# Kernel optimization log

Hardware: AMD Instinct MI355X
Metric: run time of the kernel (lower is better)

## Reference

```python
import jax, jax.numpy as jnp
import numpy as np

N, H, D, G = 8192, 512, 256, 64
TAU, LAM, ALPHA, BETA = 0.5, 0.5, 1.0, 1.0
EPS_G, EPS_L = 1e-6, 1e-5


def setup_inputs() -> dict:
    key = jax.random.key(0)
    ks = jax.random.split(key, 8)
    za = jax.random.normal(ks[0], (N, H), dtype=jnp.float32)
    zb = jax.random.normal(ks[1], (N, H), dtype=jnp.float32)
    pos = jax.random.uniform(ks[2], (N, N), dtype=jnp.float32)
    batch = (jnp.arange(N, dtype=jnp.int32) * G) // N  # sorted, covers all G groups
    s_h = np.sqrt(2.0 / H).astype(np.float32)  # kaiming fan_in relu
    W1 = jax.random.normal(ks[3], (H, H), dtype=jnp.float32) * s_h
    b1 = jnp.zeros((H,), dtype=jnp.float32)
    W2 = jax.random.normal(ks[4], (H, H), dtype=jnp.float32) * s_h
    b2 = jnp.zeros((H,), dtype=jnp.float32)
    W3 = jax.random.normal(ks[5], (H, D), dtype=jnp.float32) * s_h
    b3 = jnp.zeros((D,), dtype=jnp.float32)
    a1 = jnp.full((1,), 0.5, dtype=jnp.float32)
    g1 = jnp.ones((H,), dtype=jnp.float32)
    be1 = jnp.zeros((H,), dtype=jnp.float32)
    a2 = jnp.full((1,), 0.5, dtype=jnp.float32)
    g2 = jnp.ones((H,), dtype=jnp.float32)
    be2 = jnp.zeros((H,), dtype=jnp.float32)
    return {"za": za, "zb": zb, "pos": pos, "batch": batch,
            "W1": W1, "b1": b1, "a1": a1, "g1": g1, "be1": be1,
            "W2": W2, "b2": b2, "a2": a2, "g2": g2, "be2": be2,
            "W3": W3, "b3": b3}


def _project(z, W1, b1, a1, g1, be1, W2, b2, a2, g2, be2, W3, b3):
    h = z @ W1 + b1
    h = jnp.tanh(a1 * h) * g1 + be1  # DyT
    h = h @ W2 + b2
    h = jnp.tanh(a2 * h) * g2 + be2  # DyT
    p = h @ W3 + b3
    return p * jax.nn.sigmoid(p)  # z1_proj * sigmoid(z1_proj)


def reference(za, zb, pos, batch, W1, b1, a1, g1, be1, W2, b2, a2, g2, be2, W3, b3):
    za_p = _project(za, W1, b1, a1, g1, be1, W2, b2, a2, g2, be2, W3, b3)
    zb_p = _project(zb, W1, b1, a1, g1, be1, W2, b2, a2, g2, be2, W3, b3)

    # exp(cosine / tau): same matrix used by global_contrast (sim) and local_contrast
    na = jnp.linalg.norm(za_p, axis=-1, keepdims=True)  # [N,1]
    nb = jnp.linalg.norm(zb_p, axis=-1, keepdims=True)  # [N,1]
    m = jnp.exp((za_p @ zb_p.T) / (na * nb.T) / TAU)    # [N,N]

    # global contrast
    a2b = m / (jnp.sum(m, axis=1, keepdims=True) + EPS_G)
    lori_a = -jnp.mean(jnp.log(jnp.sum(a2b * pos, axis=-1)))
    b2a = m.T
    b2a = b2a / (jnp.sum(b2a, axis=1, keepdims=True) + EPS_G)
    lori_b = -jnp.mean(jnp.log(jnp.sum(b2a * pos, axis=-1)))
    global_loss = LAM * lori_a + (1.0 - LAM) * lori_b

    # local contrast: per-group sums via one-hot matmul (replaces O(G^2) mask loop)
    pos_sim = jnp.diagonal(m)                              # [N]
    pos_sim_graph = jax.ops.segment_sum(pos_sim, batch, num_segments=G)  # [G]
    hot = jax.nn.one_hot(batch, G, dtype=m.dtype)          # [N,G]
    batch_sim = hot.T @ m @ hot                            # [G,G]
    graph_sim = jnp.diagonal(batch_sim)
    neg0 = jnp.sum(batch_sim, axis=0) - graph_sim
    neg1 = jnp.sum(batch_sim, axis=1) - graph_sim
    loss0 = jnp.mean(jnp.log(pos_sim_graph / (neg0 + EPS_L)))
    loss1 = jnp.mean(jnp.log(pos_sim_graph / (neg1 + EPS_L)))
    inter_loss = (loss0 + loss1) / 2.0
    inner_loss = -jnp.mean(jnp.log(pos_sim_graph / (graph_sim - pos_sim_graph + EPS_L)))
    local_loss = ALPHA * inter_loss + BETA * inner_loss

    total_loss = global_loss + local_loss
    return total_loss, jnp.concatenate((za_p, zb_p), axis=1)
```

## Files before the change

kernel.cpp:

```cpp
#include <hip/hip_runtime.h>
#include <hip/hip_bf16.h>
#include <cstdint>
#include <cstddef>


typedef __bf16 bf16;
typedef __bf16 bf16x4 __attribute__((ext_vector_type(4)));
typedef __bf16 bf16x8 __attribute__((ext_vector_type(8)));
typedef float  f32x4  __attribute__((ext_vector_type(4)));

#define NROWS 8192
#define HDIM  512
#define DDIM  256
#define GGRP  64
#define INV_TAU 2.0f

__device__ __forceinline__ void async_ld16(const void* g, void* l) {
    __builtin_amdgcn_global_load_lds(
        (__attribute__((address_space(1))) void*)(g),
        (__attribute__((address_space(3))) void*)(l), 16, 0, 0);
}

__device__ __forceinline__ void mfma_tile_128(
    const bf16* __restrict__ A, const bf16* __restrict__ Bt, int K,
    int row0, int col0, bf16* ldsA, bf16* ldsB, f32x4 acc[4][4], int tid)
{
    const int lane = tid & 63;
    const int wave = tid >> 6;
    const int wrow = (wave >> 1) * 64;
    const int wcol = (wave & 1) * 64;
    const int lrow = lane & 15;
    const int lk8  = (lane >> 4) * 8;

    const int sr = tid >> 2;
    const int sc = (tid & 3) * 8;
    const bf16* gA0 = A  + (size_t)(row0 + sr) * K + sc;
    const bf16* gA1 = gA0 + (size_t)64 * K;
    const bf16* gB0 = Bt + (size_t)(col0 + sr) * K + sc;
    const bf16* gB1 = gB0 + (size_t)64 * K;
    bf16* dA0 = ldsA + (wave * 64) * 8;
    bf16* dA1 = ldsA + (256 + wave * 64) * 8;
    bf16* dB0 = ldsB + (wave * 64) * 8;
    bf16* dB1 = ldsB + (256 + wave * 64) * 8;

#pragma unroll
    for (int i = 0; i < 4; i++)
#pragma unroll
        for (int j = 0; j < 4; j++) acc[i][j] = (f32x4){0.f, 0.f, 0.f, 0.f};

    for (int k0 = 0; k0 < K; k0 += 32) {
        async_ld16(gA0, dA0); async_ld16(gA1, dA1);
        async_ld16(gB0, dB0); async_ld16(gB1, dB1);
        gA0 += 32; gA1 += 32; gB0 += 32; gB1 += 32;
        __syncthreads();

        bf16x8 af[4], bfr[4];
#pragma unroll
        for (int fi = 0; fi < 4; fi++)
            af[fi] = *(const bf16x8*)(ldsA + (wrow + fi * 16 + lrow) * 32 + lk8);
#pragma unroll
        for (int fj = 0; fj < 4; fj++)
            bfr[fj] = *(const bf16x8*)(ldsB + (wcol + fj * 16 + lrow) * 32 + lk8);
#pragma unroll
        for (int fi = 0; fi < 4; fi++)
#pragma unroll
            for (int fj = 0; fj < 4; fj++)
                acc[fi][fj] = __builtin_amdgcn_mfma_f32_16x16x32_bf16(
                    af[fi], bfr[fj], acc[fi][fj], 0, 0, 0);
        __syncthreads();
    }
}

__global__ __launch_bounds__(256) void gemm_dyt(
    const bf16* __restrict__ A, const bf16* __restrict__ Bt, bf16* __restrict__ C,
    int K, int N,
    const float* __restrict__ bias, const float* __restrict__ alph,
    const float* __restrict__ gam, const float* __restrict__ bet)
{
    __shared__ __align__(16) bf16 ldsA[128 * 32];
    __shared__ __align__(16) bf16 ldsB[128 * 32];
    f32x4 acc[4][4];
    const int row0 = blockIdx.y * 128, col0 = blockIdx.x * 128;
    mfma_tile_128(A, Bt, K, row0, col0, ldsA, ldsB, acc, threadIdx.x);

    const int lane = threadIdx.x & 63, wave = threadIdx.x >> 6;
    const int wrow = (wave >> 1) * 64, wcol = (wave & 1) * 64;
    const int lcol = lane & 15, lrg = (lane >> 4) * 4;
    const float a = alph[0];
#pragma unroll
    for (int fi = 0; fi < 4; fi++) {
        const int rbase = row0 + wrow + fi * 16 + lrg;
#pragma unroll
        for (int fj = 0; fj < 4; fj++) {
            const int cg = col0 + wcol + fj * 16 + lcol;
            const float bcol = bias[cg], gcol = gam[cg], becol = bet[cg];
#pragma unroll
            for (int r = 0; r < 4; r++) {
                float x = acc[fi][fj][r] + bcol;
                float y = tanhf(a * x) * gcol + becol;
                C[(size_t)(rbase + r) * N + cg] = (bf16)y;
            }
        }
    }
}

__global__ __launch_bounds__(256) void gemm_silu(
    const bf16* __restrict__ A, const bf16* __restrict__ Bt,
    bf16* __restrict__ P16, float* __restrict__ out1, float* __restrict__ n2,
    const float* __restrict__ bias)
{
    __shared__ __align__(16) bf16 ldsA[128 * 32];
    __shared__ __align__(16) bf16 ldsB[128 * 32];
    f32x4 acc[4][4];
    const int row0 = blockIdx.y * 128, col0 = blockIdx.x * 128;
    mfma_tile_128(A, Bt, 512, row0, col0, ldsA, ldsB, acc, threadIdx.x);

    const int lane = threadIdx.x & 63, wave = threadIdx.x >> 6;
    const int wrow = (wave >> 1) * 64, wcol = (wave & 1) * 64;
    const int lcol = lane & 15, lrg = (lane >> 4) * 4;

    float nacc[4][4];
#pragma unroll
    for (int i = 0; i < 4; i++)
#pragma unroll
        for (int r = 0; r < 4; r++) nacc[i][r] = 0.f;

#pragma unroll
    for (int fi = 0; fi < 4; fi++) {
        const int rbase = row0 + wrow + fi * 16 + lrg;
#pragma unroll
        for (int fj = 0; fj < 4; fj++) {
            const int cg = col0 + wcol + fj * 16 + lcol;
            const float bcol = bias[cg];
#pragma unroll
            for (int r = 0; r < 4; r++) {
                const int rg = rbase + r;
                float x = acc[fi][fj][r] + bcol;
                float y = x / (1.f + __expf(-x));
                P16[(size_t)rg * 256 + cg] = (bf16)y;
                size_t oidx = (rg < NROWS) ? ((size_t)rg * 512 + cg)
                                           : ((size_t)(rg - NROWS) * 512 + 256 + cg);
                out1[oidx] = y;
                nacc[fi][r] += y * y;
            }
        }
    }
#pragma unroll
    for (int fi = 0; fi < 4; fi++)
#pragma unroll
        for (int r = 0; r < 4; r++) {
            float v = nacc[fi][r];
            v += __shfl_xor(v, 1); v += __shfl_xor(v, 2);
            v += __shfl_xor(v, 4); v += __shfl_xor(v, 8);
            if (lcol == 0)
                atomicAdd(&n2[row0 + wrow + fi * 16 + lrg + r], v);
        }
}

template <int PASS1>
__global__ __launch_bounds__(256, 2) void sim_pass(
    const bf16* __restrict__ PA, const bf16* __restrict__ PB,
    const float* __restrict__ rnA, const float* __restrict__ rnB,
    const float* __restrict__ pos,
    float* __restrict__ rsum, float* __restrict__ wsum,
    float* __restrict__ bsim, float* __restrict__ psg)
{
    __shared__ __align__(16) bf16  ldsA[128 * 32];
    __shared__ __align__(16) bf16  ldsB[128 * 32];
    __shared__ __align__(16) float ldsP[128 * 128];

    const int tid  = threadIdx.x;
    const int lane = tid & 63, wave = tid >> 6;
    const int wrow = (wave >> 1) * 64, wcol = (wave & 1) * 64;
    const int lrow = lane & 15, lk8 = (lane >> 4) * 8;
    const int I = blockIdx.y, J = blockIdx.x;
    const int row0 = I * 128, col0 = J * 128;

    const int sr = tid >> 2, sc = (tid & 3) * 8;
    const bf16* gA0 = PA + (size_t)(row0 + sr) * DDIM + sc;
    const bf16* gA1 = gA0 + (size_t)64 * DDIM;
    const bf16* gB0 = PB + (size_t)(col0 + sr) * DDIM + sc;
    const bf16* gB1 = gB0 + (size_t)64 * DDIM;
    bf16* dA0 = ldsA + (wave * 64) * 8;
    bf16* dA1 = ldsA + (256 + wave * 64) * 8;
    bf16* dB0 = ldsB + (wave * 64) * 8;
    bf16* dB1 = ldsB + (256 + wave * 64) * 8;

    const int pr0 = tid >> 5;
    const int pc0 = (tid & 31) * 4;
    const float* gP0 = pos + (size_t)(row0 + pr0) * NROWS + col0 + pc0;
    const float* gP1 = gP0 + (size_t)8 * NROWS;
    float* dP = ldsP + wave * 256;

    f32x4 acc[4][4];
#pragma unroll
    for (int i = 0; i < 4; i++)
#pragma unroll
        for (int j = 0; j < 4; j++) acc[i][j] = (f32x4){0.f, 0.f, 0.f, 0.f};

    for (int it = 0; it < 8; ++it) {
        async_ld16(gA0, dA0); async_ld16(gA1, dA1);
        async_ld16(gB0, dB0); async_ld16(gB1, dB1);
        async_ld16(gP0, dP);  async_ld16(gP1, dP + 1024);
        gA0 += 32; gA1 += 32; gB0 += 32; gB1 += 32;
        gP0 += (size_t)16 * NROWS; gP1 += (size_t)16 * NROWS; dP += 2048;
        __syncthreads();

        bf16x8 af[4], bfr[4];
#pragma unroll
        for (int fi = 0; fi < 4; fi++)
            af[fi] = *(const bf16x8*)(ldsA + (wrow + fi * 16 + lrow) * 32 + lk8);
#pragma unroll
        for (int fj = 0; fj < 4; fj++)
            bfr[fj] = *(const bf16x8*)(ldsB + (wcol + fj * 16 + lrow) * 32 + lk8);
#pragma unroll
        for (int fi = 0; fi < 4; fi++)
#pragma unroll
            for (int fj = 0; fj < 4; fj++)
                acc[fi][fj] = __builtin_amdgcn_mfma_f32_16x16x32_bf16(
                    af[fi], bfr[fj], acc[fi][fj], 0, 0, 0);
        __syncthreads();
    }

    const int lcol = lane & 15, lrg = (lane >> 4) * 4;
    float racc[4][4], sacc[4][4];
#pragma unroll
    for (int i = 0; i < 4; i++)
#pragma unroll
        for (int r = 0; r < 4; r++) { racc[i][r] = 0.f; sacc[i][r] = 0.f; }
    float msum = 0.f;

#pragma unroll
    for (int fi = 0; fi < 4; fi++) {
        const int rl = wrow + fi * 16 + lrg;
        const int rbase = row0 + rl;
        float rna[4];
#pragma unroll
        for (int r = 0; r < 4; r++) rna[r] = rnA[rbase + r] * INV_TAU;
#pragma unroll
        for (int fj = 0; fj < 4; fj++) {
            const int cl = wcol + fj * 16 + lcol;
            const int cg = col0 + cl;
            const float rnb = rnB[cg];
#pragma unroll
            for (int r = 0; r < 4; r++) {
                float mval = __expf(acc[fi][fj][r] * rna[r] * rnb);
                float pv = ldsP[(rl + r) * 128 + cl];
                racc[fi][r] += mval;
                sacc[fi][r] += mval * pv;
                if (PASS1) {
                    msum += mval;
                    if (I == J && (rbase + r) == cg)
                        atomicAdd(&psg[I], mval);
                }
            }
        }
    }
#pragma unroll
    for (int fi = 0; fi < 4; fi++)
#pragma unroll
        for (int r = 0; r < 4; r++) {
            float rv = racc[fi][r], sv = sacc[fi][r];
            rv += __shfl_xor(rv, 1); rv += __shfl_xor(rv, 2);
            rv += __shfl_xor(rv, 4); rv += __shfl_xor(rv, 8);
            sv += __shfl_xor(sv, 1); sv += __shfl_xor(sv, 2);
            sv += __shfl_xor(sv, 4); sv += __shfl_xor(sv, 8);
            if (lcol == 0) {
                const int rg = row0 + wrow + fi * 16 + lrg + r;
                atomicAdd(&rsum[rg], rv);
                atomicAdd(&wsum[rg], sv);
            }
        }
    if (PASS1) {
        msum += __shfl_xor(msum, 1);  msum += __shfl_xor(msum, 2);
        msum += __shfl_xor(msum, 4);  msum += __shfl_xor(msum, 8);
        msum += __shfl_xor(msum, 16); msum += __shfl_xor(msum, 32);
        if (lane == 0) atomicAdd(&bsim[I * GGRP + J], msum);
    }
}

__global__ void cast4_kernel(const float4* __restrict__ x, bf16x4* __restrict__ y, int n4)
{
    int i = blockIdx.x * blockDim.x + threadIdx.x;
    if (i < n4) {
        float4 v = x[i];
        bf16x4 o;
        o[0] = (bf16)v.x; o[1] = (bf16)v.y; o[2] = (bf16)v.z; o[3] = (bf16)v.w;
        y[i] = o;
    }
}

__global__ void transpose_cast(const float* __restrict__ W, bf16* __restrict__ Wt,
                               int R, int C)
{
    __shared__ float tile[32][33];
    const int c0 = blockIdx.x * 32, r0 = blockIdx.y * 32;
    const int tx = threadIdx.x, ty = threadIdx.y;
    for (int i = ty; i < 32; i += 8)
        tile[i][tx] = W[(size_t)(r0 + i) * C + c0 + tx];
    __syncthreads();
    for (int i = ty; i < 32; i += 8)
        Wt[(size_t)(c0 + i) * R + r0 + tx] = (bf16)tile[tx][i];
}

__global__ void rsqrt_kernel(const float* __restrict__ x, float* __restrict__ y, int n)
{
    int i = blockIdx.x * blockDim.x + threadIdx.x;
    if (i < n) y[i] = rsqrtf(fmaxf(x[i], 1e-30f));
}

__global__ __launch_bounds__(256) void loss_rows(
    const float* __restrict__ sa, const float* __restrict__ rowsum,
    const float* __restrict__ sb, const float* __restrict__ colsum,
    float* __restrict__ gsum)
{
    __shared__ float red[8];
    const int i = blockIdx.x * 256 + threadIdx.x;
    float la = __logf(sa[i] / (rowsum[i] + 1e-6f));
    float lb = __logf(sb[i] / (colsum[i] + 1e-6f));
    for (int m = 1; m < 64; m <<= 1) { la += __shfl_xor(la, m); lb += __shfl_xor(lb, m); }
    const int w = threadIdx.x >> 6;
    if ((threadIdx.x & 63) == 0) { red[w] = la; red[4 + w] = lb; }
    __syncthreads();
    if (threadIdx.x == 0)  atomicAdd(&gsum[0], red[0] + red[1] + red[2] + red[3]);
    if (threadIdx.x == 64) atomicAdd(&gsum[1], red[4] + red[5] + red[6] + red[7]);
}

__global__ void loss_final(
    const float* __restrict__ bs, const float* __restrict__ psg,
    const float* __restrict__ gsum, float* __restrict__ out)
{
    const int t = threadIdx.x;
    float c0 = 0.f, c1 = 0.f;
    for (int a = 0; a < GGRP; a++) { c0 += bs[a * GGRP + t]; c1 += bs[t * GGRP + a]; }
    const float d = bs[t * (GGRP + 1)];
    const float p = psg[t];
    float l0  = __logf(p / (c0 - d + 1e-5f));
    float l1  = __logf(p / (c1 - d + 1e-5f));
    float lin = __logf(p / (d - p + 1e-5f));
    for (int m = 1; m < 64; m <<= 1) {
        l0 += __shfl_xor(l0, m); l1 += __shfl_xor(l1, m); lin += __shfl_xor(lin, m);
    }
    if (t == 0) {
        const float lori_a = -gsum[0] / (float)NROWS;
        const float lori_b = -gsum[1] / (float)NROWS;
        const float global_loss = 0.5f * (lori_a + lori_b);
        const float inter = 0.5f * (l0 + l1) / (float)GGRP;
        const float inner = -lin / (float)GGRP;
        out[0] = global_loss + inter + inner;
    }
}

extern "C" void kernel_launch(void* const* d_in, const int* in_sizes, int n_in,
                              void* d_out, int out_size, void* d_ws, size_t ws_size,
                              hipStream_t stream)
{
    const float* za  = (const float*)d_in[0];
    const float* zb  = (const float*)d_in[1];
    const float* pos = (const float*)d_in[2];
    const float* W1  = (const float*)d_in[4];
    const float* b1  = (const float*)d_in[5];
    const float* a1  = (const float*)d_in[6];
    const float* g1  = (const float*)d_in[7];
    const float* be1 = (const float*)d_in[8];
    const float* W2  = (const float*)d_in[9];
    const float* b2  = (const float*)d_in[10];
    const float* a2  = (const float*)d_in[11];
    const float* g2  = (const float*)d_in[12];
    const float* be2 = (const float*)d_in[13];
    const float* W3  = (const float*)d_in[14];
    const float* b3  = (const float*)d_in[15];
    float* out = (float*)d_out;

    char* ws = (char*)d_ws;
    float* rowsum = (float*)(ws);
    float* colsum = rowsum + 8192;
    float* s_a    = colsum + 8192;
    float* s_b    = s_a + 8192;
    float* n2     = s_b + 8192;
    float* bsim   = n2 + 16384;
    float* psg    = bsim + 4096;
    float* gsum   = psg + 64;
    const size_t accum_bytes = (size_t)(8192 * 4 + 16384 + 4096 + 64 + 2) * 4;

    float* rn  = (float*)(ws + 213504);
    bf16* Z16  = (bf16*)(ws + 213504 + 65536);
    bf16* h1   = Z16 + (size_t)16384 * 512;
    bf16* p16  = h1 + (size_t)16384 * 512;
    bf16* W1t  = p16 + (size_t)16384 * 256;
    bf16* W2t  = W1t + (size_t)512 * 512;
    bf16* W3t  = W2t + (size_t)512 * 512;

    hipMemsetAsync(d_ws, 0, accum_bytes, stream);

    const int n4 = NROWS * HDIM / 4;
    cast4_kernel<<<n4 / 256, 256, 0, stream>>>((const float4*)za, (bf16x4*)Z16, n4);
    cast4_kernel<<<n4 / 256, 256, 0, stream>>>((const float4*)zb,
                                               (bf16x4*)(Z16 + (size_t)NROWS * HDIM), n4);
    dim3 tb(32, 8);
    transpose_cast<<<dim3(16, 16), tb, 0, stream>>>(W1, W1t, 512, 512);
    transpose_cast<<<dim3(16, 16), tb, 0, stream>>>(W2, W2t, 512, 512);
    transpose_cast<<<dim3(8, 16),  tb, 0, stream>>>(W3, W3t, 512, 256);

    gemm_dyt<<<dim3(4, 128), 256, 0, stream>>>(Z16, W1t, h1, 512, 512, b1, a1, g1, be1);
    gemm_dyt<<<dim3(4, 128), 256, 0, stream>>>(h1, W2t, Z16 , 512, 512, b2, a2, g2, be2);
    gemm_silu<<<dim3(2, 128), 256, 0, stream>>>(Z16, W3t, p16, out + 1, n2, b3);
    rsqrt_kernel<<<16384 / 256, 256, 0, stream>>>(n2, rn, 16384);

    const bf16* pa = p16;
    const bf16* pb = p16 + (size_t)NROWS * DDIM;
    sim_pass<1><<<dim3(64, 64), 256, 0, stream>>>(pa, pb, rn, rn + NROWS, pos,
                                                  rowsum, s_a, bsim, psg);
    sim_pass<0><<<dim3(64, 64), 256, 0, stream>>>(pb, pa, rn + NROWS, rn, pos,
                                                  colsum, s_b, nullptr, nullptr);

    loss_rows<<<32, 256, 0, stream>>>(s_a, rowsum, s_b, colsum, gsum);
    loss_final<<<1, 64, 0, stream>>>(bsim, psg, gsum, out);
}
```

Measured before the change: 863.2 us.

## Load pos tile directly to registers and widen sim_pass K-tiles; fuse prep kernels

sim_pass no longer stages the 128x128 fp32 pos tile through LDS. Each lane now loads its pos values straight into registers at kernel start, so the loads overlap the MFMA loop, and the 64KB LDS buffer goes away. The K loop now uses 64-wide chunks with a prefetch of the next chunk after the barrier, which halves the number of barriers. The two input cast kernels and the three weight transpose kernels are each merged into one launch to cut launch overhead. The cost is 64 extra VGPRs per thread for the pos values, which may hurt occupancy, and uncoalesced pos row loads of 16 floats per lane.

```diff
diff --git a/kernel.cpp b/kernel.cpp
--- a/kernel.cpp
+++ b/kernel.cpp
@@ -165,32 +165,23 @@
     float* __restrict__ rsum, float* __restrict__ wsum,
     float* __restrict__ bsim, float* __restrict__ psg)
 {
-    __shared__ __align__(16) bf16  ldsA[128 * 32];
-    __shared__ __align__(16) bf16  ldsB[128 * 32];
-    __shared__ __align__(16) float ldsP[128 * 128];
+    __shared__ __align__(16) bf16 ldsA[128 * 64];
+    __shared__ __align__(16) bf16 ldsB[128 * 64];
 
     const int tid  = threadIdx.x;
     const int lane = tid & 63, wave = tid >> 6;
     const int wrow = (wave >> 1) * 64, wcol = (wave & 1) * 64;
     const int lrow = lane & 15, lk8 = (lane >> 4) * 8;
+    const int lcol = lane & 15, lrg = (lane >> 4) * 4;
     const int I = blockIdx.y, J = blockIdx.x;
     const int row0 = I * 128, col0 = J * 128;
 
-    const int sr = tid >> 2, sc = (tid & 3) * 8;
-    const bf16* gA0 = PA + (size_t)(row0 + sr) * DDIM + sc;
-    const bf16* gA1 = gA0 + (size_t)64 * DDIM;
-    const bf16* gB0 = PB + (size_t)(col0 + sr) * DDIM + sc;
-    const bf16* gB1 = gB0 + (size_t)64 * DDIM;
-    bf16* dA0 = ldsA + (wave * 64) * 8;
-    bf16* dA1 = ldsA + (256 + wave * 64) * 8;
-    bf16* dB0 = ldsB + (wave * 64) * 8;
-    bf16* dB1 = ldsB + (256 + wave * 64) * 8;
-
-    const int pr0 = tid >> 5;
-    const int pc0 = (tid & 31) * 4;
-    const float* gP0 = pos + (size_t)(row0 + pr0) * NROWS + col0 + pc0;
-    const float* gP1 = gP0 + (size_t)8 * NROWS;
-    float* dP = ldsP + wave * 256;
+    const int srow = tid >> 3;
+    const int scol = (tid & 7) * 8;
+    const bf16* gA = PA + (size_t)(row0 + srow) * DDIM + scol;
+    const bf16* gB = PB + (size_t)(col0 + srow) * DDIM + scol;
+    bf16* dA = ldsA + wave * 512;
+    bf16* dB = ldsB + wave * 512;
 
     f32x4 acc[4][4];
 #pragma unroll
@@ -198,31 +189,59 @@
 #pragma unroll
         for (int j = 0; j < 4; j++) acc[i][j] = (f32x4){0.f, 0.f, 0.f, 0.f};
 
-    for (int it = 0; it < 8; ++it) {
-        async_ld16(gA0, dA0); async_ld16(gA1, dA1);
-        async_ld16(gB0, dB0); async_ld16(gB1, dB1);
-        async_ld16(gP0, dP);  async_ld16(gP1, dP + 1024);
-        gA0 += 32; gA1 += 32; gB0 += 32; gB1 += 32;
-        gP0 += (size_t)16 * NROWS; gP1 += (size_t)16 * NROWS; dP += 2048;
+#pragma unroll
+    for (int c = 0; c < 4; c++) {
+        async_ld16(gA + (size_t)c * 32 * DDIM, dA + c * 2048);
+        async_ld16(gB + (size_t)c * 32 * DDIM, dB + c * 2048);
+    }
+
+    float pv[4][4][4];
+#pragma unroll
+    for (int fi = 0; fi < 4; fi++)
+#pragma unroll
+        for (int r = 0; r < 4; r++) {
+            const float* prow = pos + (size_t)(row0 + wrow + fi * 16 + lrg + r) * NROWS
+                                    + col0 + wcol + lcol;
+#pragma unroll
+            for (int fj = 0; fj < 4; fj++) pv[fi][fj][r] = prow[fj * 16];
+        }
+#pragma unroll
+    for (int fi = 0; fi < 4; fi++)
+#pragma unroll
+        for (int fj = 0; fj < 4; fj++)
+#pragma unroll
+            for (int r = 0; r < 4; r++)
+                asm volatile("" : "+v"(pv[fi][fj][r]));
+
+    for (int k0 = 0; k0 < 256; k0 += 64) {
         __syncthreads();
-
-        bf16x8 af[4], bfr[4];
-#pragma unroll
-        for (int fi = 0; fi < 4; fi++)
-            af[fi] = *(const bf16x8*)(ldsA + (wrow + fi * 16 + lrow) * 32 + lk8);
-#pragma unroll
-        for (int fj = 0; fj < 4; fj++)
-            bfr[fj] = *(const bf16x8*)(ldsB + (wcol + fj * 16 + lrow) * 32 + lk8);
-#pragma unroll
-        for (int fi = 0; fi < 4; fi++)
+#pragma unroll
+        for (int s = 0; s < 2; s++) {
+            bf16x8 af[4], bfr[4];
+#pragma unroll
+            for (int fi = 0; fi < 4; fi++)
+                af[fi] = *(const bf16x8*)(ldsA + (wrow + fi * 16 + lrow) * 64 + s * 32 + lk8);
 #pragma unroll
             for (int fj = 0; fj < 4; fj++)
-                acc[fi][fj] = __builtin_amdgcn_mfma_f32_16x16x32_bf16(
-                    af[fi], bfr[fj], acc[fi][fj], 0, 0, 0);
+                bfr[fj] = *(const bf16x8*)(ldsB + (wcol + fj * 16 + lrow) * 64 + s * 32 + lk8);
+#pragma unroll
+            for (int fi = 0; fi < 4; fi++)
+#pragma unroll
+                for (int fj = 0; fj < 4; fj++)
+                    acc[fi][fj] = __builtin_amdgcn_mfma_f32_16x16x32_bf16(
+                        af[fi], bfr[fj], acc[fi][fj], 0, 0, 0);
+        }
         __syncthreads();
-    }
-
-    const int lcol = lane & 15, lrg = (lane >> 4) * 4;
+        if (k0 < 192) {
+            const int kn = k0 + 64;
+#pragma unroll
+            for (int c = 0; c < 4; c++) {
+                async_ld16(gA + (size_t)c * 32 * DDIM + kn, dA + c * 2048);
+                async_ld16(gB + (size_t)c * 32 * DDIM + kn, dB + c * 2048);
+            }
+        }
+    }
+
     float racc[4][4], sacc[4][4];
 #pragma unroll
     for (int i = 0; i < 4; i++)
@@ -232,22 +251,19 @@
 
 #pragma unroll
     for (int fi = 0; fi < 4; fi++) {
-        const int rl = wrow + fi * 16 + lrg;
-        const int rbase = row0 + rl;
+        const int rbase = row0 + wrow + fi * 16 + lrg;
         float rna[4];
 #pragma unroll
         for (int r = 0; r < 4; r++) rna[r] = rnA[rbase + r] * INV_TAU;
 #pragma unroll
         for (int fj = 0; fj < 4; fj++) {
-            const int cl = wcol + fj * 16 + lcol;
-            const int cg = col0 + cl;
+            const int cg = col0 + wcol + fj * 16 + lcol;
             const float rnb = rnB[cg];
 #pragma unroll
             for (int r = 0; r < 4; r++) {
                 float mval = __expf(acc[fi][fj][r] * rna[r] * rnb);
-                float pv = ldsP[(rl + r) * 128 + cl];
                 racc[fi][r] += mval;
-                sacc[fi][r] += mval * pv;
+                sacc[fi][r] += mval * pv[fi][fj][r];
                 if (PASS1) {
                     msum += mval;
                     if (I == J && (rbase + r) == cg)
@@ -279,28 +295,34 @@
     }
 }
 
-__global__ void cast4_kernel(const float4* __restrict__ x, bf16x4* __restrict__ y, int n4)
+__global__ void cast_both_kernel(const float4* __restrict__ xa,
+                                 const float4* __restrict__ xb,
+                                 bf16x4* __restrict__ y, int n4)
 {
     int i = blockIdx.x * blockDim.x + threadIdx.x;
-    if (i < n4) {
-        float4 v = x[i];
-        bf16x4 o;
-        o[0] = (bf16)v.x; o[1] = (bf16)v.y; o[2] = (bf16)v.z; o[3] = (bf16)v.w;
-        y[i] = o;
-    }
-}
-
-__global__ void transpose_cast(const float* __restrict__ W, bf16* __restrict__ Wt,
-                               int R, int C)
+    float4 v = (i < n4) ? xa[i] : xb[i - n4];
+    bf16x4 o;
+    o[0] = (bf16)v.x; o[1] = (bf16)v.y; o[2] = (bf16)v.z; o[3] = (bf16)v.w;
+    y[i] = o;
+}
+
+__global__ void transpose_cast3(const float* __restrict__ W1, bf16* __restrict__ W1t,
+                                const float* __restrict__ W2, bf16* __restrict__ W2t,
+                                const float* __restrict__ W3, bf16* __restrict__ W3t)
 {
     __shared__ float tile[32][33];
+    const int z = blockIdx.z;
+    const float* W = (z == 0) ? W1 : (z == 1) ? W2 : W3;
+    bf16* Wt = (z == 0) ? W1t : (z == 1) ? W2t : W3t;
+    const int C = (z == 2) ? 256 : 512;
     const int c0 = blockIdx.x * 32, r0 = blockIdx.y * 32;
+    if (c0 >= C) return;
     const int tx = threadIdx.x, ty = threadIdx.y;
     for (int i = ty; i < 32; i += 8)
         tile[i][tx] = W[(size_t)(r0 + i) * C + c0 + tx];
     __syncthreads();
     for (int i = ty; i < 32; i += 8)
-        Wt[(size_t)(c0 + i) * R + r0 + tx] = (bf16)tile[tx][i];
+        Wt[(size_t)(c0 + i) * 512 + r0 + tx] = (bf16)tile[tx][i];
 }
 
 __global__ void rsqrt_kernel(const float* __restrict__ x, float* __restrict__ y, int n)
@@ -394,13 +416,10 @@
     hipMemsetAsync(d_ws, 0, accum_bytes, stream);
 
     const int n4 = NROWS * HDIM / 4;
-    cast4_kernel<<<n4 / 256, 256, 0, stream>>>((const float4*)za, (bf16x4*)Z16, n4);
-    cast4_kernel<<<n4 / 256, 256, 0, stream>>>((const float4*)zb,
-                                               (bf16x4*)(Z16 + (size_t)NROWS * HDIM), n4);
-    dim3 tb(32, 8);
-    transpose_cast<<<dim3(16, 16), tb, 0, stream>>>(W1, W1t, 512, 512);
-    transpose_cast<<<dim3(16, 16), tb, 0, stream>>>(W2, W2t, 512, 512);
-    transpose_cast<<<dim3(8, 16),  tb, 0, stream>>>(W3, W3t, 512, 256);
+    cast_both_kernel<<<2 * n4 / 256, 256, 0, stream>>>(
+        (const float4*)za, (const float4*)zb, (bf16x4*)Z16, n4);
+    transpose_cast3<<<dim3(16, 16, 3), dim3(32, 8), 0, stream>>>(
+        W1, W1t, W2, W2t, W3, W3t);
 
     gemm_dyt<<<dim3(4, 128), 256, 0, stream>>>(Z16, W1t, h1, 512, 512, b1, a1, g1, be1);
     gemm_dyt<<<dim3(4, 128), 256, 0, stream>>>(h1, W2t, Z16 , 512, 512, b2, a2, g2, be2);
```

Result: faster. 837.1 us (-3.0%).
